# Optimization experiments

Hardware: AMD Instinct MI355X
Metric: run time of the kernel (lower is better)

## Reference

```python
import jax, jax.numpy as jnp
import numpy as np

B, T = 256, 64          # batch, rollout length
D, S, A, E, H = 1024, 64, 32, 1024, 1024  # deter, stoch, action, obs_embed, hidden


def setup_inputs() -> dict:
    key = jax.random.key(0)
    ks = jax.random.split(key, 12)
    f32 = jnp.float32

    def w(k, shape, fan_in):
        return (jax.random.normal(k, shape, f32) / np.float32(np.sqrt(fan_in)))

    return dict(
        obs_embeds=jax.random.normal(ks[0], (B, T, E), f32),
        action_embs=jax.random.normal(ks[1], (B, T, A), f32),
        noise_prior=jax.random.normal(ks[2], (T - 1, B, S), f32),  # randn_like in prior
        noise_post=jax.random.normal(ks[3], (T - 1, B, S), f32),   # randn_like in posterior
        # fc_state_action_embed: Linear(S+A -> D)
        W_sa=w(ks[4], (D, S + A), S + A), b_sa=jnp.zeros((D,), f32),
        # GRUCell(D, D): torch layout [3D, D] with gate order r, z, n
        W_ih=w(ks[5], (3 * D, D), D), b_ih=jnp.zeros((3 * D,), f32),
        W_hh=w(ks[6], (3 * D, D), D), b_hh=jnp.zeros((3 * D,), f32),
        # state_prior: Linear(D->H), ELU, Linear(H->2S)
        Wp1=w(ks[7], (H, D), D), bp1=jnp.zeros((H,), f32),
        Wp2=w(ks[8], (2 * S, H), H), bp2=jnp.zeros((2 * S,), f32),
        # state_posterior: Linear(D+E->H), ELU, Linear(H->2S)
        Wq1=w(ks[9], (H, D + E), D + E), bq1=jnp.zeros((H,), f32),
        Wq2=w(ks[10], (2 * S, H), H), bq2=jnp.zeros((2 * S,), f32),
    )


def reference(obs_embeds, action_embs, noise_prior, noise_post,
              W_sa, b_sa, W_ih, b_ih, W_hh, b_hh,
              Wp1, bp1, Wp2, bp2, Wq1, bq1, Wq2, bq2):
    # observe_rollout: init state is zeros; step t uses obs[:, t+1], action[:, t].
    b = obs_embeds.shape[0]
    h0 = jnp.zeros((b, D), obs_embeds.dtype)
    s0 = jnp.zeros((b, S), obs_embeds.dtype)
    obs_seq = jnp.swapaxes(obs_embeds[:, 1:], 0, 1)   # [T-1, B, E]
    act_seq = jnp.swapaxes(action_embs[:, :-1], 0, 1)  # [T-1, B, A]

    def step(carry, xs):
        h, s = carry  # posterior deter / stoch state from previous step
        obs, act, ep, eq = xs
        # prior: embed (stoch, action) -> GRU update
        e = jax.nn.elu(jnp.concatenate([s, act], -1) @ W_sa.T + b_sa)
        gi = e @ W_ih.T + b_ih
        gh = h @ W_hh.T + b_hh
        ir, iz, ia = jnp.split(gi, 3, axis=-1)
        hr, hz, ha = jnp.split(gh, 3, axis=-1)
        r = jax.nn.sigmoid(ir + hr)
        z = jax.nn.sigmoid(iz + hz)
        n = jnp.tanh(ia + r * ha)
        h_new = (1.0 - z) * n + z * h  # prior deter state
        # prior dist + reparam sample
        pm = jax.nn.elu(h_new @ Wp1.T + bp1) @ Wp2.T + bp2
        pmean, pstd = jnp.split(pm, 2, axis=-1)
        pstd = jax.nn.softplus(pstd) + 0.1
        pstoch = pmean + pstd * ep
        # posterior dist + reparam sample (conditioned on h_new and obs)
        qm = jax.nn.elu(jnp.concatenate([h_new, obs], -1) @ Wq1.T + bq1) @ Wq2.T + bq2
        qmean, qstd = jnp.split(qm, 2, axis=-1)
        qstd = jax.nn.softplus(qstd) + 0.1
        qstoch = qmean + qstd * eq
        out = jnp.concatenate([h_new, pmean, pstd, pstoch, qmean, qstd, qstoch], -1)
        return (h_new, qstoch), out

    _, outs = jax.lax.scan(step, (h0, s0), (obs_seq, act_seq, noise_prior, noise_post))
    # outs: [T-1, B, D + 6S] = (prior deter, prior mean/std/stoch, post mean/std/stoch)
    return outs
```

## Files before the change

### kernel.cpp

```cpp
#include <hip/hip_runtime.h>

typedef __attribute__((ext_vector_type(8))) short short8;
typedef __attribute__((ext_vector_type(4))) float f32x4;

#define OSTEP (256*1408)

#define OFF_WIH  ((size_t)0)
#define OFF_WHH  ((size_t)3145728)
#define OFF_WP1  ((size_t)6291456)
#define OFF_WQ1  ((size_t)7340032)
#define OFF_WP2  ((size_t)9437184)
#define OFF_WQ2  ((size_t)9568256)
#define OFF_HBF0 ((size_t)9699328)
#define OFF_HBF1 ((size_t)9961472)
#define OFF_EBF  ((size_t)10223616)
#define OFF_P1E  ((size_t)10485760)
#define OFF_Q1E  ((size_t)10747904)
#define F32_BYTE_OFF ((size_t)22020096)

__device__ __forceinline__ unsigned short f2bf(float f){
  union { float f; unsigned u; } v; v.f = f;
  unsigned u = v.u;
  u += 0x7fffu + ((u >> 16) & 1u);
  return (unsigned short)(u >> 16);
}
__device__ __forceinline__ float sigf(float x){ return 1.0f/(1.0f+__expf(-x)); }
__device__ __forceinline__ float tanhf_(float x){
  float e = __expf(-2.0f*fabsf(x));
  float t = (1.0f-e)/(1.0f+e);
  return x>=0.f ? t : -t;
}
__device__ __forceinline__ float eluf(float x){ return x>0.f ? x : __expf(x)-1.0f; }
__device__ __forceinline__ float softplusf(float x){ return x>20.f ? x : log1pf(__expf(x)); }
__device__ __forceinline__ short8 ld8(const unsigned short* p){ return *(const short8*)p; }

__global__ void k_prep(const float* __restrict__ wih, const float* __restrict__ whh,
                       const float* __restrict__ wp1, const float* __restrict__ wq1,
                       const float* __restrict__ wp2, const float* __restrict__ wq2,
                       unsigned short* __restrict__ dst){
  size_t i4 = ((size_t)blockIdx.x*256 + threadIdx.x)*4;
  const size_t total = 9699328;
  if(i4 >= total) return;
  const float* src; size_t off;
  if(i4 < 3145728){ src=wih; off=0; }
  else if(i4 < 6291456){ src=whh; off=3145728; }
  else if(i4 < 7340032){ src=wp1; off=6291456; }
  else if(i4 < 9437184){ src=wq1; off=7340032; }
  else if(i4 < 9568256){ src=wp2; off=9437184; }
  else { src=wq2; off=9568256; }
  size_t j = i4 - off;
  float4 v = *(const float4*)(src + j);
  unsigned long long p = (unsigned long long)f2bf(v.x)
                       | ((unsigned long long)f2bf(v.y) << 16)
                       | ((unsigned long long)f2bf(v.z) << 32)
                       | ((unsigned long long)f2bf(v.w) << 48);
  *(unsigned long long*)(dst + i4) = p;
}

__global__ __launch_bounds__(384) void k_gru(
    const unsigned short* __restrict__ e_bf,
    const unsigned short* __restrict__ h_bf,
    const unsigned short* __restrict__ wih_bf,
    const unsigned short* __restrict__ whh_bf,
    const float* __restrict__ b_ih, const float* __restrict__ b_hh,
    const float* __restrict__ hprev, int hprev_ld,
    float* __restrict__ out_t,
    unsigned short* __restrict__ hnext_bf)
{
  int bx = blockIdx.x, by = blockIdx.y;
  int tid = threadIdx.x, w = tid >> 6, lane = tid & 63;
  int g = w % 3; bool isI = (w < 3);
  const unsigned short* A  = isI ? e_bf  : h_bf;
  const unsigned short* Bw = isI ? wih_bf : whh_bf;
  int brow = g*1024 + bx*32;
  int arow = by*32;
  int l15 = lane & 15, q8 = (lane >> 4)*8;

  f32x4 z4 = {0.f,0.f,0.f,0.f};
  f32x4 acc00=z4, acc01=z4, acc10=z4, acc11=z4;

  const unsigned short* pa0 = A  + (size_t)(arow + l15)*1024 + q8;
  const unsigned short* pa1 = pa0 + 16*1024;
  const unsigned short* pb0 = Bw + (size_t)(brow + l15)*1024 + q8;
  const unsigned short* pb1 = pb0 + 16*1024;

  #pragma unroll 4
  for(int kk=0; kk<1024; kk+=32){
    short8 a0 = ld8(pa0+kk), a1 = ld8(pa1+kk);
    short8 b0 = ld8(pb0+kk), b1 = ld8(pb1+kk);
    acc00 = __builtin_amdgcn_mfma_f32_16x16x32_bf16(a0,b0,acc00,0,0,0);
    acc01 = __builtin_amdgcn_mfma_f32_16x16x32_bf16(a0,b1,acc01,0,0,0);
    acc10 = __builtin_amdgcn_mfma_f32_16x16x32_bf16(a1,b0,acc10,0,0,0);
    acc11 = __builtin_amdgcn_mfma_f32_16x16x32_bf16(a1,b1,acc11,0,0,0);
  }

  __shared__ float sg[6][32][33];
  int rr = (lane>>4)*4;
  #pragma unroll
  for(int v=0; v<4; v++){
    sg[w][0 +rr+v][0 +l15] = acc00[v];
    sg[w][0 +rr+v][16+l15] = acc01[v];
    sg[w][16+rr+v][0 +l15] = acc10[v];
    sg[w][16+rr+v][16+l15] = acc11[v];
  }
  __syncthreads();

  for(int i=tid; i<1024; i+=384){
    int m = i>>5, n = i&31;
    int d = bx*32+n, b = by*32+m;
    float ir = sg[0][m][n] + b_ih[d];
    float iz = sg[1][m][n] + b_ih[1024+d];
    float ia = sg[2][m][n] + b_ih[2048+d];
    float hr = sg[3][m][n] + b_hh[d];
    float hz = sg[4][m][n] + b_hh[1024+d];
    float ha = sg[5][m][n] + b_hh[2048+d];
    float r = sigf(ir+hr), zz = sigf(iz+hz);
    float nn = tanhf_(ia + r*ha);
    float hold = hprev[(size_t)b*hprev_ld + d];
    float hnew = (1.f-zz)*nn + zz*hold;
    out_t[(size_t)b*1408 + d] = hnew;
    hnext_bf[(size_t)b*1024 + d] = f2bf(hnew);
  }
}

__global__ __launch_bounds__(256) void k_heads1(
    const unsigned short* __restrict__ hnew_bf,
    const float* __restrict__ obs, int tcol,
    const unsigned short* __restrict__ wp1_bf,
    const unsigned short* __restrict__ wq1_bf,
    const float* __restrict__ bp1, const float* __restrict__ bq1,
    unsigned short* __restrict__ p1e, unsigned short* __restrict__ q1e)
{
  int bx = blockIdx.x, by = blockIdx.y;
  bool isQ = (bx >= 32); int nt = bx & 31;
  int tid = threadIdx.x, w = tid>>6, lane = tid&63;
  int mi = w & 1, ni = w >> 1;
  int l15 = lane & 15, q8 = (lane>>4)*8;
  int arowg = by*32 + mi*16 + l15;
  int browg = nt*32 + ni*16 + l15;

  f32x4 acc = {0.f,0.f,0.f,0.f};
  const unsigned short* pa = hnew_bf + (size_t)arowg*1024 + q8;

  if(!isQ){
    const unsigned short* pb = wp1_bf + (size_t)browg*1024 + q8;
    #pragma unroll 4
    for(int kk=0; kk<1024; kk+=32){
      acc = __builtin_amdgcn_mfma_f32_16x16x32_bf16(ld8(pa+kk), ld8(pb+kk), acc,0,0,0);
    }
  } else {
    const unsigned short* pb = wq1_bf + (size_t)browg*2048 + q8;
    #pragma unroll 4
    for(int kk=0; kk<1024; kk+=32){
      acc = __builtin_amdgcn_mfma_f32_16x16x32_bf16(ld8(pa+kk), ld8(pb+kk), acc,0,0,0);
    }
    const float* obsrow = obs + ((size_t)arowg*64 + tcol)*1024 + q8;
    #pragma unroll 4
    for(int kk=0; kk<1024; kk+=32){
      const float4* f = (const float4*)(obsrow + kk);
      float4 x0 = f[0], x1 = f[1];
      short8 a;
      a[0]=(short)f2bf(x0.x); a[1]=(short)f2bf(x0.y); a[2]=(short)f2bf(x0.z); a[3]=(short)f2bf(x0.w);
      a[4]=(short)f2bf(x1.x); a[5]=(short)f2bf(x1.y); a[6]=(short)f2bf(x1.z); a[7]=(short)f2bf(x1.w);
      acc = __builtin_amdgcn_mfma_f32_16x16x32_bf16(a, ld8(pb+1024+kk), acc,0,0,0);
    }
  }

  const float* bias = isQ ? bq1 : bp1;
  unsigned short* dst = isQ ? q1e : p1e;
  int col = browg;
  float bv = bias[col];
  #pragma unroll
  for(int v=0; v<4; v++){
    int b = by*32 + mi*16 + (lane>>4)*4 + v;
    float val = eluf(acc[v] + bv);
    dst[(size_t)b*1024 + col] = f2bf(val);
  }
}

__global__ __launch_bounds__(256) void k_heads2(
    const unsigned short* __restrict__ p1e, const unsigned short* __restrict__ q1e,
    const unsigned short* __restrict__ wp2_bf, const unsigned short* __restrict__ wq2_bf,
    const float* __restrict__ bp2, const float* __restrict__ bq2,
    float* __restrict__ pm, float* __restrict__ qm)
{
  int bx = blockIdx.x, by = blockIdx.y;
  int col0 = bx*32; bool isQ = (col0 >= 128); int c0 = col0 & 127;
  int tid = threadIdx.x, w = tid>>6, lane = tid&63;
  int mi = w & 1, ni = w >> 1;
  int l15 = lane & 15, q8 = (lane>>4)*8;
  const unsigned short* A  = isQ ? q1e : p1e;
  const unsigned short* Bw = isQ ? wq2_bf : wp2_bf;
  const float* bias = isQ ? bq2 : bp2;
  float* outb = isQ ? qm : pm;

  int arowg = by*32 + mi*16 + l15;
  int browg = c0 + ni*16 + l15;
  f32x4 acc = {0.f,0.f,0.f,0.f};
  const unsigned short* pa = A  + (size_t)arowg*1024 + q8;
  const unsigned short* pb = Bw + (size_t)browg*1024 + q8;
  #pragma unroll 4
  for(int kk=0; kk<1024; kk+=32){
    acc = __builtin_amdgcn_mfma_f32_16x16x32_bf16(ld8(pa+kk), ld8(pb+kk), acc,0,0,0);
  }
  float bv = bias[browg];
  #pragma unroll
  for(int v=0; v<4; v++){
    int b = by*32 + mi*16 + (lane>>4)*4 + v;
    outb[(size_t)b*128 + browg] = acc[v] + bv;
  }
}

__global__ __launch_bounds__(256) void k_sample_e(
    int t_out, int t_act,
    const float* __restrict__ pm, const float* __restrict__ qm,
    const float* __restrict__ noise_p, const float* __restrict__ noise_q,
    const float* __restrict__ act, const float* __restrict__ w_sa,
    const float* __restrict__ b_sa,
    float* __restrict__ out, unsigned short* __restrict__ e_bf)
{
  __shared__ float qst[32*64];
  __shared__ float sact[32*32];
  int bx = blockIdx.x, by = blockIdx.y, tid = threadIdx.x;

  if(t_out >= 0){
    float* out_t = out + (size_t)t_out*OSTEP;
    for(int i=tid; i<2048; i+=256){
      int m = i>>6, s = i&63; int b = by*32+m;
      float qmean = qm[(size_t)b*128 + s];
      float qstd  = softplusf(qm[(size_t)b*128 + 64 + s]) + 0.1f;
      float qs = qmean + qstd * noise_q[((size_t)t_out*256 + b)*64 + s];
      qst[m*64+s] = qs;
      if(bx == 0){
        float pmean = pm[(size_t)b*128 + s];
        float pstd  = softplusf(pm[(size_t)b*128 + 64 + s]) + 0.1f;
        float ps = pmean + pstd * noise_p[((size_t)t_out*256 + b)*64 + s];
        float* o = out_t + (size_t)b*1408;
        o[1024+s] = pmean; o[1088+s] = pstd; o[1152+s] = ps;
        o[1216+s] = qmean; o[1280+s] = qstd; o[1344+s] = qs;
      }
    }
  } else {
    for(int i=tid; i<2048; i+=256) qst[i] = 0.f;
  }
  for(int i=tid; i<1024; i+=256){
    int m = i>>5, k = i&31;
    sact[i] = act[((size_t)(by*32+m)*64 + t_act)*32 + k];
  }
  __syncthreads();

  int n = tid & 31, mb = tid >> 5;
  int d = bx*32 + n;
  const float* wrow = w_sa + (size_t)d*96;
  float a0=b_sa[d], a1=a0, a2=a0, a3=a0;
  for(int k=0; k<64; k++){
    float wv = wrow[k];
    a0 += qst[(mb+ 0)*64+k]*wv;
    a1 += qst[(mb+ 8)*64+k]*wv;
    a2 += qst[(mb+16)*64+k]*wv;
    a3 += qst[(mb+24)*64+k]*wv;
  }
  for(int k=0; k<32; k++){
    float wv = wrow[64+k];
    a0 += sact[(mb+ 0)*32+k]*wv;
    a1 += sact[(mb+ 8)*32+k]*wv;
    a2 += sact[(mb+16)*32+k]*wv;
    a3 += sact[(mb+24)*32+k]*wv;
  }
  e_bf[(size_t)(by*32+mb+ 0)*1024 + d] = f2bf(eluf(a0));
  e_bf[(size_t)(by*32+mb+ 8)*1024 + d] = f2bf(eluf(a1));
  e_bf[(size_t)(by*32+mb+16)*1024 + d] = f2bf(eluf(a2));
  e_bf[(size_t)(by*32+mb+24)*1024 + d] = f2bf(eluf(a3));
}

extern "C" void kernel_launch(void* const* d_in, const int* in_sizes, int n_in,
                              void* d_out, int out_size, void* d_ws, size_t ws_size,
                              hipStream_t stream) {
  const float* obs = (const float*)d_in[0];
  const float* act = (const float*)d_in[1];
  const float* np_ = (const float*)d_in[2];
  const float* nq_ = (const float*)d_in[3];
  const float* wsa = (const float*)d_in[4];
  const float* bsa = (const float*)d_in[5];
  const float* wih = (const float*)d_in[6];
  const float* bih = (const float*)d_in[7];
  const float* whh = (const float*)d_in[8];
  const float* bhh = (const float*)d_in[9];
  const float* wp1 = (const float*)d_in[10];
  const float* bp1 = (const float*)d_in[11];
  const float* wp2 = (const float*)d_in[12];
  const float* bp2 = (const float*)d_in[13];
  const float* wq1 = (const float*)d_in[14];
  const float* bq1 = (const float*)d_in[15];
  const float* wq2 = (const float*)d_in[16];
  const float* bq2 = (const float*)d_in[17];
  float* out = (float*)d_out;

  unsigned short* wsb = (unsigned short*)d_ws;
  unsigned short* wihb = wsb + OFF_WIH;
  unsigned short* whhb = wsb + OFF_WHH;
  unsigned short* wp1b = wsb + OFF_WP1;
  unsigned short* wq1b = wsb + OFF_WQ1;
  unsigned short* wp2b = wsb + OFF_WP2;
  unsigned short* wq2b = wsb + OFF_WQ2;
  unsigned short* hbf0 = wsb + OFF_HBF0;
  unsigned short* hbf1 = wsb + OFF_HBF1;
  unsigned short* ebf  = wsb + OFF_EBF;
  unsigned short* p1e  = wsb + OFF_P1E;
  unsigned short* q1e  = wsb + OFF_Q1E;
  float* f32b = (float*)((char*)d_ws + F32_BYTE_OFF);
  float* h0 = f32b;
  float* pm = f32b + 262144;
  float* qm = f32b + 262144 + 32768;

  hipMemsetAsync(hbf0, 0, 262144*2, stream);
  hipMemsetAsync(h0, 0, 262144*4, stream);

  k_prep<<<9472, 256, 0, stream>>>(wih, whh, wp1, wq1, wp2, wq2, wsb);

  k_sample_e<<<dim3(32,8), 256, 0, stream>>>(-1, 0, pm, qm, np_, nq_, act, wsa, bsa, out, ebf);

  for(int t=0; t<63; t++){
    const unsigned short* hb = (t&1) ? hbf1 : hbf0;
    unsigned short* hbn      = (t&1) ? hbf0 : hbf1;
    const float* hprev = t ? (out + (size_t)(t-1)*OSTEP) : h0;
    int hld = t ? 1408 : 1024;
    k_gru<<<dim3(32,8), 384, 0, stream>>>(ebf, hb, wihb, whhb, bih, bhh,
                                          hprev, hld, out + (size_t)t*OSTEP, hbn);
    k_heads1<<<dim3(64,8), 256, 0, stream>>>(hbn, obs, t+1, wp1b, wq1b, bp1, bq1, p1e, q1e);
    k_heads2<<<dim3(8,8), 256, 0, stream>>>(p1e, q1e, wp2b, wq2b, bp2, bq2, pm, qm);
    k_sample_e<<<dim3(32,8), 256, 0, stream>>>(t, t+1, pm, qm, np_, nq_, act, wsa, bsa, out, ebf);
  }
}
```

Measured before the change: 5.976 ms.

## Fuse rollout into a persistent cooperative kernel with grid-wide syncs

Replaces the per-timestep launches of four kernels (about 250 launches plus prep and memsets) with one persistent cooperative kernel of 256 blocks. Each step runs the GRU, head layer 1, head layer 2 and the sampling/embed phases separated by grid.sync() calls. Weight conversion and zeroing of the initial hidden state are folded into the same kernel. This removes launch overhead and inter-kernel gaps at the cost of grid barriers and a fixed block-to-work mapping, and it falls back to the old multi-kernel path if the cooperative launch fails.

```diff
diff --git a/kernel.cpp b/kernel.cpp
--- a/kernel.cpp
+++ b/kernel.cpp
@@ -1,4 +1,7 @@
 #include <hip/hip_runtime.h>
+#include <hip/hip_cooperative_groups.h>
+
+namespace cg = cooperative_groups;
 
 typedef __attribute__((ext_vector_type(8))) short short8;
 typedef __attribute__((ext_vector_type(4))) float f32x4;
@@ -33,6 +36,296 @@
 __device__ __forceinline__ float eluf(float x){ return x>0.f ? x : __expf(x)-1.0f; }
 __device__ __forceinline__ float softplusf(float x){ return x>20.f ? x : log1pf(__expf(x)); }
 __device__ __forceinline__ short8 ld8(const unsigned short* p){ return *(const short8*)p; }
+
+
+__device__ __forceinline__ void phaseA(
+    int blk, int tid,
+    const unsigned short* __restrict__ e_bf,
+    const unsigned short* __restrict__ h_bf,
+    const unsigned short* __restrict__ wih_bf,
+    const unsigned short* __restrict__ whh_bf,
+    const float* __restrict__ b_ih, const float* __restrict__ b_hh,
+    const float* __restrict__ hprev,
+    float* __restrict__ out_t,
+    unsigned short* __restrict__ hnext_bf,
+    float* sm)
+{
+  float (*sg)[32][33] = (float(*)[32][33])sm;
+  int bx = blk & 31, by = blk >> 5;
+  int w = tid >> 6, lane = tid & 63;
+  if (w < 6) {
+    int g = w % 3; bool isI = (w < 3);
+    const unsigned short* A  = isI ? e_bf  : h_bf;
+    const unsigned short* Bw = isI ? wih_bf : whh_bf;
+    int brow = g*1024 + bx*32;
+    int arow = by*32;
+    int l15 = lane & 15, q8 = (lane >> 4)*8;
+    f32x4 z4 = {0.f,0.f,0.f,0.f};
+    f32x4 acc00=z4, acc01=z4, acc10=z4, acc11=z4;
+    const unsigned short* pa0 = A  + (size_t)(arow + l15)*1024 + q8;
+    const unsigned short* pa1 = pa0 + 16*1024;
+    const unsigned short* pb0 = Bw + (size_t)(brow + l15)*1024 + q8;
+    const unsigned short* pb1 = pb0 + 16*1024;
+    #pragma unroll 4
+    for(int kk=0; kk<1024; kk+=32){
+      short8 a0 = ld8(pa0+kk), a1 = ld8(pa1+kk);
+      short8 b0 = ld8(pb0+kk), b1 = ld8(pb1+kk);
+      acc00 = __builtin_amdgcn_mfma_f32_16x16x32_bf16(a0,b0,acc00,0,0,0);
+      acc01 = __builtin_amdgcn_mfma_f32_16x16x32_bf16(a0,b1,acc01,0,0,0);
+      acc10 = __builtin_amdgcn_mfma_f32_16x16x32_bf16(a1,b0,acc10,0,0,0);
+      acc11 = __builtin_amdgcn_mfma_f32_16x16x32_bf16(a1,b1,acc11,0,0,0);
+    }
+    int rr = (lane>>4)*4;
+    #pragma unroll
+    for(int v=0; v<4; v++){
+      sg[w][0 +rr+v][0 +l15] = acc00[v];
+      sg[w][0 +rr+v][16+l15] = acc01[v];
+      sg[w][16+rr+v][0 +l15] = acc10[v];
+      sg[w][16+rr+v][16+l15] = acc11[v];
+    }
+  }
+  __syncthreads();
+  for(int i=tid; i<1024; i+=512){
+    int m = i>>5, n = i&31;
+    int d = bx*32+n, b = by*32+m;
+    float ir = sg[0][m][n] + b_ih[d];
+    float iz = sg[1][m][n] + b_ih[1024+d];
+    float ia = sg[2][m][n] + b_ih[2048+d];
+    float hr = sg[3][m][n] + b_hh[d];
+    float hz = sg[4][m][n] + b_hh[1024+d];
+    float ha = sg[5][m][n] + b_hh[2048+d];
+    float r = sigf(ir+hr), zz = sigf(iz+hz);
+    float nn = tanhf_(ia + r*ha);
+    float hold = hprev ? hprev[(size_t)b*1408 + d] : 0.f;
+    float hnew = (1.f-zz)*nn + zz*hold;
+    out_t[(size_t)b*1408 + d] = hnew;
+    hnext_bf[(size_t)b*1024 + d] = f2bf(hnew);
+  }
+}
+
+__device__ __forceinline__ void phaseB(
+    int blk, int tid,
+    const unsigned short* __restrict__ hnew_bf,
+    const float* __restrict__ obs, int tcol,
+    const unsigned short* __restrict__ wp1_bf,
+    const unsigned short* __restrict__ wq1_bf,
+    const float* __restrict__ bp1, const float* __restrict__ bq1,
+    unsigned short* __restrict__ p1e, unsigned short* __restrict__ q1e)
+{
+  int w = tid >> 6, lane = tid & 63;
+  int vb = blk*2 + (w>>2);
+  int bx = vb & 63, by = vb >> 6;
+  bool isQ = (bx >= 32); int nt = bx & 31;
+  int w4 = w & 3;
+  int mi = w4 & 1, ni = w4 >> 1;
+  int l15 = lane & 15, q8 = (lane>>4)*8;
+  int arowg = by*32 + mi*16 + l15;
+  int browg = nt*32 + ni*16 + l15;
+
+  f32x4 acc = {0.f,0.f,0.f,0.f};
+  const unsigned short* pa = hnew_bf + (size_t)arowg*1024 + q8;
+
+  if(!isQ){
+    const unsigned short* pb = wp1_bf + (size_t)browg*1024 + q8;
+    #pragma unroll 4
+    for(int kk=0; kk<1024; kk+=32){
+      acc = __builtin_amdgcn_mfma_f32_16x16x32_bf16(ld8(pa+kk), ld8(pb+kk), acc,0,0,0);
+    }
+  } else {
+    const unsigned short* pb = wq1_bf + (size_t)browg*2048 + q8;
+    #pragma unroll 4
+    for(int kk=0; kk<1024; kk+=32){
+      acc = __builtin_amdgcn_mfma_f32_16x16x32_bf16(ld8(pa+kk), ld8(pb+kk), acc,0,0,0);
+    }
+    const float* obsrow = obs + ((size_t)arowg*64 + tcol)*1024 + q8;
+    #pragma unroll 4
+    for(int kk=0; kk<1024; kk+=32){
+      const float4* f = (const float4*)(obsrow + kk);
+      float4 x0 = f[0], x1 = f[1];
+      short8 a;
+      a[0]=(short)f2bf(x0.x); a[1]=(short)f2bf(x0.y); a[2]=(short)f2bf(x0.z); a[3]=(short)f2bf(x0.w);
+      a[4]=(short)f2bf(x1.x); a[5]=(short)f2bf(x1.y); a[6]=(short)f2bf(x1.z); a[7]=(short)f2bf(x1.w);
+      acc = __builtin_amdgcn_mfma_f32_16x16x32_bf16(a, ld8(pb+1024+kk), acc,0,0,0);
+    }
+  }
+
+  const float* bias = isQ ? bq1 : bp1;
+  unsigned short* dst = isQ ? q1e : p1e;
+  int col = browg;
+  float bv = bias[col];
+  #pragma unroll
+  for(int v=0; v<4; v++){
+    int b = by*32 + mi*16 + (lane>>4)*4 + v;
+    float val = eluf(acc[v] + bv);
+    dst[(size_t)b*1024 + col] = f2bf(val);
+  }
+}
+
+__device__ __forceinline__ void phaseC(
+    int blk, int tid,
+    const unsigned short* __restrict__ p1e, const unsigned short* __restrict__ q1e,
+    const unsigned short* __restrict__ wp2_bf, const unsigned short* __restrict__ wq2_bf,
+    const float* __restrict__ bp2, const float* __restrict__ bq2,
+    float* __restrict__ pm, float* __restrict__ qm)
+{
+  if (tid >= 64) return;
+  int by = blk >> 5, bx = (blk >> 2) & 7, w4 = blk & 3;
+  int lane = tid;
+  int col0 = bx*32; bool isQ = (col0 >= 128); int c0 = col0 & 127;
+  int mi = w4 & 1, ni = w4 >> 1;
+  int l15 = lane & 15, q8 = (lane>>4)*8;
+  const unsigned short* A  = isQ ? q1e : p1e;
+  const unsigned short* Bw = isQ ? wq2_bf : wp2_bf;
+  const float* bias = isQ ? bq2 : bp2;
+  float* outb = isQ ? qm : pm;
+
+  int arowg = by*32 + mi*16 + l15;
+  int browg = c0 + ni*16 + l15;
+  f32x4 acc = {0.f,0.f,0.f,0.f};
+  const unsigned short* pa = A  + (size_t)arowg*1024 + q8;
+  const unsigned short* pb = Bw + (size_t)browg*1024 + q8;
+  #pragma unroll 4
+  for(int kk=0; kk<1024; kk+=32){
+    acc = __builtin_amdgcn_mfma_f32_16x16x32_bf16(ld8(pa+kk), ld8(pb+kk), acc,0,0,0);
+  }
+  float bv = bias[browg];
+  #pragma unroll
+  for(int v=0; v<4; v++){
+    int b = by*32 + mi*16 + (lane>>4)*4 + v;
+    outb[(size_t)b*128 + browg] = acc[v] + bv;
+  }
+}
+
+__device__ __forceinline__ void phaseD(
+    int t_out, int t_act, int blk, int tid,
+    const float* __restrict__ pm, const float* __restrict__ qm,
+    const float* __restrict__ noise_p, const float* __restrict__ noise_q,
+    const float* __restrict__ act, const float* __restrict__ w_sa,
+    const float* __restrict__ b_sa,
+    float* __restrict__ out, unsigned short* __restrict__ e_bf,
+    float* sm)
+{
+  float* qst  = sm;
+  float* sact = sm + 2048;
+  int bx = blk & 31, by = blk >> 5;
+
+  if(t_out >= 0){
+    float* out_t = out + (size_t)t_out*OSTEP;
+    for(int i=tid; i<2048; i+=512){
+      int m = i>>6, s = i&63; int b = by*32+m;
+      float qmean = qm[(size_t)b*128 + s];
+      float qstd  = softplusf(qm[(size_t)b*128 + 64 + s]) + 0.1f;
+      float qs = qmean + qstd * noise_q[((size_t)t_out*256 + b)*64 + s];
+      qst[m*64+s] = qs;
+      if(bx == 0){
+        float pmean = pm[(size_t)b*128 + s];
+        float pstd  = softplusf(pm[(size_t)b*128 + 64 + s]) + 0.1f;
+        float ps = pmean + pstd * noise_p[((size_t)t_out*256 + b)*64 + s];
+        float* o = out_t + (size_t)b*1408;
+        o[1024+s] = pmean; o[1088+s] = pstd; o[1152+s] = ps;
+        o[1216+s] = qmean; o[1280+s] = qstd; o[1344+s] = qs;
+      }
+    }
+  } else {
+    for(int i=tid; i<2048; i+=512) qst[i] = 0.f;
+  }
+  for(int i=tid; i<1024; i+=512){
+    int m = i>>5, k = i&31;
+    sact[i] = act[((size_t)(by*32+m)*64 + t_act)*32 + k];
+  }
+  __syncthreads();
+
+  int n = tid & 31, mb = tid >> 5;
+  int d = bx*32 + n;
+  const float* wrow = w_sa + (size_t)d*96;
+  float a0=b_sa[d], a1=a0;
+  for(int k=0; k<64; k++){
+    float wv = wrow[k];
+    a0 += qst[(mb+ 0)*64+k]*wv;
+    a1 += qst[(mb+16)*64+k]*wv;
+  }
+  for(int k=0; k<32; k++){
+    float wv = wrow[64+k];
+    a0 += sact[(mb+ 0)*32+k]*wv;
+    a1 += sact[(mb+16)*32+k]*wv;
+  }
+  e_bf[(size_t)(by*32+mb+ 0)*1024 + d] = f2bf(eluf(a0));
+  e_bf[(size_t)(by*32+mb+16)*1024 + d] = f2bf(eluf(a1));
+}
+
+__global__ __launch_bounds__(512, 1) void k_mega(
+    const float* __restrict__ obs, const float* __restrict__ act,
+    const float* __restrict__ np_, const float* __restrict__ nq_,
+    const float* __restrict__ wsa, const float* __restrict__ bsa,
+    const float* __restrict__ wih, const float* __restrict__ bih,
+    const float* __restrict__ whh, const float* __restrict__ bhh,
+    const float* __restrict__ wp1, const float* __restrict__ bp1,
+    const float* __restrict__ wp2, const float* __restrict__ bp2,
+    const float* __restrict__ wq1, const float* __restrict__ bq1,
+    const float* __restrict__ wq2, const float* __restrict__ bq2,
+    float* __restrict__ out, unsigned short* __restrict__ wsb)
+{
+  __shared__ float sm[6*32*33];
+  cg::grid_group grid = cg::this_grid();
+  int blk = blockIdx.x, tid = threadIdx.x;
+
+  unsigned short* wihb = wsb + OFF_WIH;
+  unsigned short* whhb = wsb + OFF_WHH;
+  unsigned short* wp1b = wsb + OFF_WP1;
+  unsigned short* wq1b = wsb + OFF_WQ1;
+  unsigned short* wp2b = wsb + OFF_WP2;
+  unsigned short* wq2b = wsb + OFF_WQ2;
+  unsigned short* hbf0 = wsb + OFF_HBF0;
+  unsigned short* hbf1 = wsb + OFF_HBF1;
+  unsigned short* ebf  = wsb + OFF_EBF;
+  unsigned short* p1e  = wsb + OFF_P1E;
+  unsigned short* q1e  = wsb + OFF_Q1E;
+  float* f32b = (float*)((char*)wsb + F32_BYTE_OFF);
+  float* pm = f32b + 262144;
+  float* qm = f32b + 262144 + 32768;
+
+  {
+    size_t gtid = (size_t)blk*512 + tid;
+    for(size_t i = gtid; i < (size_t)2424832; i += (size_t)131072){
+      size_t i4 = i*4;
+      const float* src; size_t off;
+      if(i4 < 3145728){ src=wih; off=0; }
+      else if(i4 < 6291456){ src=whh; off=3145728; }
+      else if(i4 < 7340032){ src=wp1; off=6291456; }
+      else if(i4 < 9437184){ src=wq1; off=7340032; }
+      else if(i4 < 9568256){ src=wp2; off=9437184; }
+      else { src=wq2; off=9568256; }
+      size_t j = i4 - off;
+      float4 v = *(const float4*)(src + j);
+      unsigned long long p = (unsigned long long)f2bf(v.x)
+                           | ((unsigned long long)f2bf(v.y) << 16)
+                           | ((unsigned long long)f2bf(v.z) << 32)
+                           | ((unsigned long long)f2bf(v.w) << 48);
+      *(unsigned long long*)(wsb + i4) = p;
+    }
+    if(gtid < 65536) ((unsigned long long*)(wsb + OFF_HBF0))[gtid] = 0ull;
+  }
+  phaseD(-1, 0, blk, tid, pm, qm, np_, nq_, act, wsa, bsa, out, ebf, sm);
+  grid.sync();
+
+  #pragma unroll 1
+  for(int t=0; t<63; t++){
+    const unsigned short* hb = (t&1) ? hbf1 : hbf0;
+    unsigned short* hbn      = (t&1) ? hbf0 : hbf1;
+    const float* hprev = t ? (out + (size_t)(t-1)*OSTEP) : (const float*)nullptr;
+
+    phaseA(blk, tid, ebf, hb, wihb, whhb, bih, bhh, hprev,
+           out + (size_t)t*OSTEP, hbn, sm);
+    grid.sync();
+    phaseB(blk, tid, hbn, obs, t+1, wp1b, wq1b, bp1, bq1, p1e, q1e);
+    grid.sync();
+    phaseC(blk, tid, p1e, q1e, wp2b, wq2b, bp2, bq2, pm, qm);
+    grid.sync();
+    phaseD(t, t+1, blk, tid, pm, qm, np_, nq_, act, wsa, bsa, out, ebf, sm);
+    grid.sync();
+  }
+}
+
 
 __global__ void k_prep(const float* __restrict__ wih, const float* __restrict__ whh,
                        const float* __restrict__ wp1, const float* __restrict__ wq1,
@@ -295,8 +588,20 @@
   const float* wq2 = (const float*)d_in[16];
   const float* bq2 = (const float*)d_in[17];
   float* out = (float*)d_out;
-
   unsigned short* wsb = (unsigned short*)d_ws;
+
+  void* args[] = {
+    (void*)&obs, (void*)&act, (void*)&np_, (void*)&nq_,
+    (void*)&wsa, (void*)&bsa, (void*)&wih, (void*)&bih,
+    (void*)&whh, (void*)&bhh, (void*)&wp1, (void*)&bp1,
+    (void*)&wp2, (void*)&bp2, (void*)&wq1, (void*)&bq1,
+    (void*)&wq2, (void*)&bq2, (void*)&out, (void*)&wsb
+  };
+  hipError_t err = hipLaunchCooperativeKernel((const void*)k_mega,
+                                              dim3(256), dim3(512),
+                                              args, 0, stream);
+  if (err == hipSuccess) return;
+
   unsigned short* wihb = wsb + OFF_WIH;
   unsigned short* whhb = wsb + OFF_WHH;
   unsigned short* wp1b = wsb + OFF_WP1;
@@ -317,7 +622,6 @@
   hipMemsetAsync(h0, 0, 262144*4, stream);
 
   k_prep<<<9472, 256, 0, stream>>>(wih, whh, wp1, wq1, wp2, wq2, wsb);
-
   k_sample_e<<<dim3(32,8), 256, 0, stream>>>(-1, 0, pm, qm, np_, nq_, act, wsa, bsa, out, ebf);
 
   for(int t=0; t<63; t++){
```

After: 12.67 ms. 2.12x slower.

## Fuse the rollout into one persistent cooperative kernel with LDS-resident weights

Applied to the files above, without the earlier changes.

Replaces the per-timestep launches of four kernels with one cooperative persistent kernel of 256 blocks. Each block converts its slice of every weight matrix to bf16 once and keeps it in LDS for all 63 steps. Phases are separated by an atomic-counter grid barrier. This removes launch overhead and repeated global weight reads. In exchange it adds grid-wide barrier latency four times per step, gives each phase narrow per-block work, and uses a bounded spin that could break correctness if the barrier times out.

```diff
diff --git a/kernel.cpp b/kernel.cpp
--- a/kernel.cpp
+++ b/kernel.cpp
@@ -2,6 +2,7 @@
 
 typedef __attribute__((ext_vector_type(8))) short short8;
 typedef __attribute__((ext_vector_type(4))) float f32x4;
+typedef unsigned short us;
 
 #define OSTEP (256*1408)
 
@@ -18,6 +19,14 @@
 #define OFF_Q1E  ((size_t)10747904)
 #define F32_BYTE_OFF ((size_t)22020096)
 
+#define L_WAI 0
+#define L_WAH 24576
+#define L_WB  49152
+#define L_WC  73728
+#define L_WD  77824
+#define L_SCR 79488
+#define LDS_TOTAL 129664
+
 __device__ __forceinline__ unsigned short f2bf(float f){
   union { float f; unsigned u; } v; v.f = f;
   unsigned u = v.u;
@@ -32,12 +41,274 @@
 }
 __device__ __forceinline__ float eluf(float x){ return x>0.f ? x : __expf(x)-1.0f; }
 __device__ __forceinline__ float softplusf(float x){ return x>20.f ? x : log1pf(__expf(x)); }
-__device__ __forceinline__ short8 ld8(const unsigned short* p){ return *(const short8*)p; }
+__device__ __forceinline__ short8 ld8(const us* p){ return *(const short8*)p; }
+
+
+__device__ __forceinline__ void phaseA_new(
+    char* lds, int blk, int tid, int t,
+    const us* __restrict__ ebf, const us* __restrict__ hb, us* __restrict__ hbn,
+    const float* __restrict__ b_ih, const float* __restrict__ b_hh,
+    const float* __restrict__ hprev, float* __restrict__ out_t,
+    const float* __restrict__ obs, us* __restrict__ obsbf)
+{
+  int w = tid>>6, lane = tid&63;
+  int l15 = lane&15, q8 = (lane>>4)*8;
+  int xr = (l15&7)<<4;
+  const char* wbi = lds + L_WAI + l15*2048;
+  const char* wbh = lds + L_WAH + l15*2048;
+  const us* paE = ebf + (size_t)(w*32 + l15)*1024 + q8;
+  const us* paH = hb  + (size_t)(w*32 + l15)*1024 + q8;
+  f32x4 z={0.f,0.f,0.f,0.f}, aI0=z, aI1=z, aH0=z, aH1=z;
+  #pragma unroll 4
+  for(int kk=0; kk<1024; kk+=32){
+    int kb = (kk+q8)*2;
+    short8 bI = *(const short8*)(wbi + (kb^xr));
+    short8 bH = *(const short8*)(wbh + (kb^xr));
+    short8 e0 = ld8(paE+kk), e1 = ld8(paE+16384+kk);
+    short8 h0 = ld8(paH+kk), h1 = ld8(paH+16384+kk);
+    aI0 = __builtin_amdgcn_mfma_f32_16x16x32_bf16(e0,bI,aI0,0,0,0);
+    aI1 = __builtin_amdgcn_mfma_f32_16x16x32_bf16(e1,bI,aI1,0,0,0);
+    aH0 = __builtin_amdgcn_mfma_f32_16x16x32_bf16(h0,bH,aH0,0,0,0);
+    aH1 = __builtin_amdgcn_mfma_f32_16x16x32_bf16(h1,bH,aH1,0,0,0);
+  }
+  float* Gih = (float*)(lds + L_SCR);
+  float* Ghh = Gih + 16*257;
+  int rr = (lane>>4)*4;
+  #pragma unroll
+  for(int v=0; v<4; v++){
+    Gih[l15*257 + w*32 + rr + v]      = aI0[v];
+    Gih[l15*257 + w*32 + 16 + rr + v] = aI1[v];
+    Ghh[l15*257 + w*32 + rr + v]      = aH0[v];
+    Ghh[l15*257 + w*32 + 16 + rr + v] = aH1[v];
+  }
+  {
+    const float* src = obs + ((size_t)(blk*64) + (t+1))*1024;
+    us* dst = obsbf + (size_t)blk*1024;
+    for(int i=tid;i<1024;i+=512) dst[i] = f2bf(src[i]);
+  }
+  __syncthreads();
+  for(int i=tid;i<1024;i+=512){
+    int di=i>>8, b=i&255; int d=blk*4+di;
+    float ir = Gih[(di  )*257 + b] + b_ih[d];
+    float iz = Gih[(4+di)*257 + b] + b_ih[1024+d];
+    float ia = Gih[(8+di)*257 + b] + b_ih[2048+d];
+    float hr = Ghh[(di  )*257 + b] + b_hh[d];
+    float hz = Ghh[(4+di)*257 + b] + b_hh[1024+d];
+    float ha = Ghh[(8+di)*257 + b] + b_hh[2048+d];
+    float r = sigf(ir+hr), zz = sigf(iz+hz);
+    float nn = tanhf_(ia + r*ha);
+    float hold = hprev ? hprev[(size_t)b*1408 + d] : 0.f;
+    float hnew = (1.f-zz)*nn + zz*hold;
+    out_t[(size_t)b*1408 + d] = hnew;
+    hbn[(size_t)b*1024 + d] = f2bf(hnew);
+  }
+}
+
+__device__ __forceinline__ void phaseB_new(
+    char* lds, int blk, int tid,
+    const us* __restrict__ hbn, const us* __restrict__ obsbf,
+    const float* __restrict__ bp1, const float* __restrict__ bq1,
+    us* __restrict__ p1e, us* __restrict__ q1e)
+{
+  int w=tid>>6, lane=tid&63, l15=lane&15, q8=(lane>>4)*8, xr=(l15&7)<<4;
+  const char* wb = lds + L_WB + l15*2048;
+  const us* paH = hbn   + (size_t)(w*32+l15)*1024 + q8;
+  const us* paO = obsbf + (size_t)(w*32+l15)*1024 + q8;
+  f32x4 z={0.f,0.f,0.f,0.f}, c10=z,c11=z,c20=z,c21=z;
+  #pragma unroll 4
+  for(int kk=0;kk<1024;kk+=32){
+    int kb=(kk+q8)*2;
+    short8 bw = *(const short8*)(wb + (kb^xr));
+    c10 = __builtin_amdgcn_mfma_f32_16x16x32_bf16(ld8(paH+kk),       bw, c10,0,0,0);
+    c11 = __builtin_amdgcn_mfma_f32_16x16x32_bf16(ld8(paH+16384+kk), bw, c11,0,0,0);
+    c20 = __builtin_amdgcn_mfma_f32_16x16x32_bf16(ld8(paO+kk),       bw, c20,0,0,0);
+    c21 = __builtin_amdgcn_mfma_f32_16x16x32_bf16(ld8(paO+16384+kk), bw, c21,0,0,0);
+  }
+  float* G1 = (float*)(lds+L_SCR); float* G2 = G1 + 16*257;
+  int rr=(lane>>4)*4;
+  #pragma unroll
+  for(int v=0;v<4;v++){
+    G1[l15*257 + w*32 + rr + v]      = c10[v];
+    G1[l15*257 + w*32 + 16 + rr + v] = c11[v];
+    G2[l15*257 + w*32 + rr + v]      = c20[v];
+    G2[l15*257 + w*32 + 16 + rr + v] = c21[v];
+  }
+  __syncthreads();
+  for(int i=tid;i<1024;i+=512){
+    int ci=i>>8, b=i&255; int c=blk*4+ci;
+    float p1 = eluf(G1[ci*257+b] + bp1[c]);
+    float q1 = eluf(G1[(4+ci)*257+b] + G2[(8+ci)*257+b] + bq1[c]);
+    p1e[(size_t)b*1024+c]=f2bf(p1);
+    q1e[(size_t)b*1024+c]=f2bf(q1);
+  }
+}
+
+__device__ __forceinline__ void phaseC_new(
+    char* lds, int blk, int tid, int t,
+    const us* __restrict__ p1e, const us* __restrict__ q1e,
+    const float* __restrict__ bp2, const float* __restrict__ bq2,
+    const float* __restrict__ np_, const float* __restrict__ nq_,
+    float* __restrict__ out_t, float* __restrict__ qstg)
+{
+  int w=tid>>6, lane=tid&63, l15=lane&15, q8=(lane>>4)*8, xr=(l15&7)<<4;
+  int kind = blk>>7, idx=blk&127, s=idx>>1, bh=idx&1, b0=bh*128;
+  const us* A = kind ? q1e : p1e;
+  const char* wc = lds + L_WC + l15*2048;
+  const us* pa = A + (size_t)(b0 + w*16 + l15)*1024 + q8;
+  f32x4 c0={0.f,0.f,0.f,0.f};
+  #pragma unroll 4
+  for(int kk=0;kk<1024;kk+=32){
+    int kb=(kk+q8)*2;
+    c0 = __builtin_amdgcn_mfma_f32_16x16x32_bf16(ld8(pa+kk), *(const short8*)(wc+(kb^xr)), c0,0,0,0);
+  }
+  float* Gc=(float*)(lds+L_SCR);
+  int rr=(lane>>4)*4;
+  #pragma unroll
+  for(int v=0;v<4;v++) Gc[l15*129 + w*16 + rr + v] = c0[v];
+  __syncthreads();
+  const float* b2 = kind? bq2 : bp2;
+  const float* nz = kind? nq_ : np_;
+  if(tid<128){
+    int b=tid, bg=b0+b;
+    float mean = Gc[0*129+b] + b2[s];
+    float stdv = softplusf(Gc[1*129+b] + b2[64+s]) + 0.1f;
+    float st = mean + stdv * nz[((size_t)t*256+bg)*64 + s];
+    float* o = out_t + (size_t)bg*1408 + (kind?1216:1024);
+    o[s]=mean; o[64+s]=stdv; o[128+s]=st;
+    if(kind) qstg[(size_t)bg*64+s]=st;
+  }
+}
+
+__device__ __forceinline__ void phaseD_new(
+    char* lds, int blk, int tid, int t_out, int t_act,
+    const float* __restrict__ qstg, const float* __restrict__ act,
+    const float* __restrict__ b_sa, us* __restrict__ ebf)
+{
+  float* wd  = (float*)(lds + L_WD);
+  float* qld = (float*)(lds + L_SCR);
+  float* ald = qld + 128*65;
+  int dl = tid>>7, b = tid&127;
+  int d = blk*4 + dl;
+  float bias = b_sa[d];
+  for(int ch=0; ch<2; ch++){
+    int B0 = ch*128;
+    if(t_out>=0){
+      for(int i=tid;i<8192;i+=512){int bb=i>>6,k=i&63; qld[bb*65+k]=qstg[(size_t)(B0+bb)*64+k];}
+    } else {
+      for(int i=tid;i<8192;i+=512){int bb=i>>6,k=i&63; qld[bb*65+k]=0.f;}
+    }
+    for(int i=tid;i<4096;i+=512){int bb=i>>5,k=i&31; ald[bb*33+k]=act[((size_t)(B0+bb)*64 + t_act)*32 + k];}
+    __syncthreads();
+    float a = bias;
+    for(int k=0;k<64;k++) a += qld[b*65+k]*wd[dl*96+k];
+    for(int k=0;k<32;k++) a += ald[b*33+k]*wd[dl*96+64+k];
+    ebf[(size_t)(B0+b)*1024 + d] = f2bf(eluf(a));
+    __syncthreads();
+  }
+}
+
+__global__ __launch_bounds__(512, 1) void k_mega(
+    const float* __restrict__ obs, const float* __restrict__ act,
+    const float* __restrict__ np_, const float* __restrict__ nq_,
+    const float* __restrict__ wsa, const float* __restrict__ bsa,
+    const float* __restrict__ wih, const float* __restrict__ bih,
+    const float* __restrict__ whh, const float* __restrict__ bhh,
+    const float* __restrict__ wp1, const float* __restrict__ bp1,
+    const float* __restrict__ wp2, const float* __restrict__ bp2,
+    const float* __restrict__ wq1, const float* __restrict__ bq1,
+    const float* __restrict__ wq2, const float* __restrict__ bq2,
+    float* __restrict__ out, us* __restrict__ wsb)
+{
+  extern __shared__ char lds[];
+  int blk = blockIdx.x, tid = threadIdx.x;
+
+  us* obsbf = wsb + OFF_WIH;
+  us* hbf0  = wsb + OFF_HBF0;
+  us* hbf1  = wsb + OFF_HBF1;
+  us* ebf   = wsb + OFF_EBF;
+  us* p1e   = wsb + OFF_P1E;
+  us* q1e   = wsb + OFF_Q1E;
+  float* f32b = (float*)((char*)wsb + F32_BYTE_OFF);
+  unsigned* cnt = (unsigned*)f32b;
+  float* qstg = f32b + 8192;
+
+  unsigned ep = 0;
+  #define GBAR() do{ __syncthreads(); ++ep; \
+    if(tid==0){ \
+      __hip_atomic_fetch_add(cnt,1u,__ATOMIC_RELEASE,__HIP_MEMORY_SCOPE_AGENT); \
+      unsigned _it=0; \
+      while(__hip_atomic_load(cnt,__ATOMIC_RELAXED,__HIP_MEMORY_SCOPE_AGENT) < ep*256u \
+            && _it<65536u){ ++_it; __builtin_amdgcn_s_sleep(2); } \
+      (void)__hip_atomic_load(cnt,__ATOMIC_ACQUIRE,__HIP_MEMORY_SCOPE_AGENT); \
+    } \
+    __syncthreads(); }while(0)
+
+  for(int i=tid; i<12*512; i+=512){
+    int r=i>>9, kp=(i&511)*2;
+    int srow = (r>>2)*1024 + blk*4 + (r&3);
+    float2 vI = *(const float2*)(wih + (size_t)srow*1024 + kp);
+    float2 vH = *(const float2*)(whh + (size_t)srow*1024 + kp);
+    unsigned pI = (unsigned)f2bf(vI.x) | ((unsigned)f2bf(vI.y)<<16);
+    unsigned pH = (unsigned)f2bf(vH.x) | ((unsigned)f2bf(vH.y)<<16);
+    int off = r*2048 + ((kp*2)^((r&7)<<4));
+    *(unsigned*)(lds + L_WAI + off) = pI;
+    *(unsigned*)(lds + L_WAH + off) = pH;
+  }
+  for(int i=tid; i<12*512; i+=512){
+    int r=i>>9, kp=(i&511)*2;
+    const float* src;
+    if(r<4)      src = wp1 + (size_t)(blk*4+r)*1024 + kp;
+    else if(r<8) src = wq1 + (size_t)(blk*4+r-4)*2048 + kp;
+    else         src = wq1 + (size_t)(blk*4+r-8)*2048 + 1024 + kp;
+    float2 v = *(const float2*)src;
+    unsigned p = (unsigned)f2bf(v.x) | ((unsigned)f2bf(v.y)<<16);
+    *(unsigned*)(lds + L_WB + r*2048 + ((kp*2)^((r&7)<<4))) = p;
+  }
+  {
+    int kind=blk>>7, s=(blk&127)>>1;
+    const float* W2 = kind? wq2 : wp2;
+    for(int i=tid; i<2*512; i+=512){
+      int r=i>>9, kp=(i&511)*2;
+      float2 v = *(const float2*)(W2 + (size_t)((r?64:0)+s)*1024 + kp);
+      unsigned p = (unsigned)f2bf(v.x) | ((unsigned)f2bf(v.y)<<16);
+      *(unsigned*)(lds + L_WC + r*2048 + ((kp*2)^((r&7)<<4))) = p;
+    }
+  }
+  for(int i=tid;i<384;i+=512){
+    int r=i/96, k=i-r*96;
+    ((float*)(lds+L_WD))[r*96+k] = wsa[(size_t)(blk*4+r)*96 + k];
+  }
+  { unsigned long long* p=(unsigned long long*)hbf0;
+    for(int i=tid;i<256;i+=512) p[(size_t)blk*256+i]=0ull; }
+  __syncthreads();
+
+  phaseD_new(lds, blk, tid, -1, 0, qstg, act, bsa, ebf);
+  GBAR();
+
+  #pragma unroll 1
+  for(int t=0; t<63; t++){
+    const us* hb = (t&1) ? hbf1 : hbf0;
+    us* hbn      = (t&1) ? hbf0 : hbf1;
+    const float* hprev = t ? (out + (size_t)(t-1)*OSTEP) : (const float*)nullptr;
+    float* out_t = out + (size_t)t*OSTEP;
+
+    phaseA_new(lds, blk, tid, t, ebf, hb, hbn, bih, bhh, hprev, out_t, obs, obsbf);
+    GBAR();
+    phaseB_new(lds, blk, tid, hbn, obsbf, bp1, bq1, p1e, q1e);
+    GBAR();
+    phaseC_new(lds, blk, tid, t, p1e, q1e, bp2, bq2, np_, nq_, out_t, qstg);
+    GBAR();
+    phaseD_new(lds, blk, tid, t, t+1, qstg, act, bsa, ebf);
+    GBAR();
+  }
+  #undef GBAR
+}
+
 
 __global__ void k_prep(const float* __restrict__ wih, const float* __restrict__ whh,
                        const float* __restrict__ wp1, const float* __restrict__ wq1,
                        const float* __restrict__ wp2, const float* __restrict__ wq2,
-                       unsigned short* __restrict__ dst){
+                       us* __restrict__ dst){
   size_t i4 = ((size_t)blockIdx.x*256 + threadIdx.x)*4;
   const size_t total = 9699328;
   if(i4 >= total) return;
@@ -58,20 +329,17 @@
 }
 
 __global__ __launch_bounds__(384) void k_gru(
-    const unsigned short* __restrict__ e_bf,
-    const unsigned short* __restrict__ h_bf,
-    const unsigned short* __restrict__ wih_bf,
-    const unsigned short* __restrict__ whh_bf,
+    const us* __restrict__ e_bf, const us* __restrict__ h_bf,
+    const us* __restrict__ wih_bf, const us* __restrict__ whh_bf,
     const float* __restrict__ b_ih, const float* __restrict__ b_hh,
     const float* __restrict__ hprev, int hprev_ld,
-    float* __restrict__ out_t,
-    unsigned short* __restrict__ hnext_bf)
+    float* __restrict__ out_t, us* __restrict__ hnext_bf)
 {
   int bx = blockIdx.x, by = blockIdx.y;
   int tid = threadIdx.x, w = tid >> 6, lane = tid & 63;
   int g = w % 3; bool isI = (w < 3);
-  const unsigned short* A  = isI ? e_bf  : h_bf;
-  const unsigned short* Bw = isI ? wih_bf : whh_bf;
+  const us* A  = isI ? e_bf  : h_bf;
+  const us* Bw = isI ? wih_bf : whh_bf;
   int brow = g*1024 + bx*32;
   int arow = by*32;
   int l15 = lane & 15, q8 = (lane >> 4)*8;
@@ -79,10 +347,10 @@
   f32x4 z4 = {0.f,0.f,0.f,0.f};
   f32x4 acc00=z4, acc01=z4, acc10=z4, acc11=z4;
 
-  const unsigned short* pa0 = A  + (size_t)(arow + l15)*1024 + q8;
-  const unsigned short* pa1 = pa0 + 16*1024;
-  const unsigned short* pb0 = Bw + (size_t)(brow + l15)*1024 + q8;
-  const unsigned short* pb1 = pb0 + 16*1024;
+  const us* pa0 = A  + (size_t)(arow + l15)*1024 + q8;
+  const us* pa1 = pa0 + 16*1024;
+  const us* pb0 = Bw + (size_t)(brow + l15)*1024 + q8;
+  const us* pb1 = pb0 + 16*1024;
 
   #pragma unroll 4
   for(int kk=0; kk<1024; kk+=32){
@@ -124,12 +392,11 @@
 }
 
 __global__ __launch_bounds__(256) void k_heads1(
-    const unsigned short* __restrict__ hnew_bf,
+    const us* __restrict__ hnew_bf,
     const float* __restrict__ obs, int tcol,
-    const unsigned short* __restrict__ wp1_bf,
-    const unsigned short* __restrict__ wq1_bf,
+    const us* __restrict__ wp1_bf, const us* __restrict__ wq1_bf,
     const float* __restrict__ bp1, const float* __restrict__ bq1,
-    unsigned short* __restrict__ p1e, unsigned short* __restrict__ q1e)
+    us* __restrict__ p1e, us* __restrict__ q1e)
 {
   int bx = blockIdx.x, by = blockIdx.y;
   bool isQ = (bx >= 32); int nt = bx & 31;
@@ -140,16 +407,16 @@
   int browg = nt*32 + ni*16 + l15;
 
   f32x4 acc = {0.f,0.f,0.f,0.f};
-  const unsigned short* pa = hnew_bf + (size_t)arowg*1024 + q8;
+  const us* pa = hnew_bf + (size_t)arowg*1024 + q8;
 
   if(!isQ){
-    const unsigned short* pb = wp1_bf + (size_t)browg*1024 + q8;
+    const us* pb = wp1_bf + (size_t)browg*1024 + q8;
     #pragma unroll 4
     for(int kk=0; kk<1024; kk+=32){
       acc = __builtin_amdgcn_mfma_f32_16x16x32_bf16(ld8(pa+kk), ld8(pb+kk), acc,0,0,0);
     }
   } else {
-    const unsigned short* pb = wq1_bf + (size_t)browg*2048 + q8;
+    const us* pb = wq1_bf + (size_t)browg*2048 + q8;
     #pragma unroll 4
     for(int kk=0; kk<1024; kk+=32){
       acc = __builtin_amdgcn_mfma_f32_16x16x32_bf16(ld8(pa+kk), ld8(pb+kk), acc,0,0,0);
@@ -167,7 +434,7 @@
   }
 
   const float* bias = isQ ? bq1 : bp1;
-  unsigned short* dst = isQ ? q1e : p1e;
+  us* dst = isQ ? q1e : p1e;
   int col = browg;
   float bv = bias[col];
   #pragma unroll
@@ -179,8 +446,8 @@
 }
 
 __global__ __launch_bounds__(256) void k_heads2(
-    const unsigned short* __restrict__ p1e, const unsigned short* __restrict__ q1e,
-    const unsigned short* __restrict__ wp2_bf, const unsigned short* __restrict__ wq2_bf,
+    const us* __restrict__ p1e, const us* __restrict__ q1e,
+    const us* __restrict__ wp2_bf, const us* __restrict__ wq2_bf,
     const float* __restrict__ bp2, const float* __restrict__ bq2,
     float* __restrict__ pm, float* __restrict__ qm)
 {
@@ -189,16 +456,16 @@
   int tid = threadIdx.x, w = tid>>6, lane = tid&63;
   int mi = w & 1, ni = w >> 1;
   int l15 = lane & 15, q8 = (lane>>4)*8;
-  const unsigned short* A  = isQ ? q1e : p1e;
-  const unsigned short* Bw = isQ ? wq2_bf : wp2_bf;
+  const us* A  = isQ ? q1e : p1e;
+  const us* Bw = isQ ? wq2_bf : wp2_bf;
   const float* bias = isQ ? bq2 : bp2;
   float* outb = isQ ? qm : pm;
 
   int arowg = by*32 + mi*16 + l15;
   int browg = c0 + ni*16 + l15;
   f32x4 acc = {0.f,0.f,0.f,0.f};
-  const unsigned short* pa = A  + (size_t)arowg*1024 + q8;
-  const unsigned short* pb = Bw + (size_t)browg*1024 + q8;
+  const us* pa = A  + (size_t)arowg*1024 + q8;
+  const us* pb = Bw + (size_t)browg*1024 + q8;
   #pragma unroll 4
   for(int kk=0; kk<1024; kk+=32){
     acc = __builtin_amdgcn_mfma_f32_16x16x32_bf16(ld8(pa+kk), ld8(pb+kk), acc,0,0,0);
@@ -217,7 +484,7 @@
     const float* __restrict__ noise_p, const float* __restrict__ noise_q,
     const float* __restrict__ act, const float* __restrict__ w_sa,
     const float* __restrict__ b_sa,
-    float* __restrict__ out, unsigned short* __restrict__ e_bf)
+    float* __restrict__ out, us* __restrict__ e_bf)
 {
   __shared__ float qst[32*64];
   __shared__ float sact[32*32];
@@ -295,19 +562,41 @@
   const float* wq2 = (const float*)d_in[16];
   const float* bq2 = (const float*)d_in[17];
   float* out = (float*)d_out;
-
-  unsigned short* wsb = (unsigned short*)d_ws;
-  unsigned short* wihb = wsb + OFF_WIH;
-  unsigned short* whhb = wsb + OFF_WHH;
-  unsigned short* wp1b = wsb + OFF_WP1;
-  unsigned short* wq1b = wsb + OFF_WQ1;
-  unsigned short* wp2b = wsb + OFF_WP2;
-  unsigned short* wq2b = wsb + OFF_WQ2;
-  unsigned short* hbf0 = wsb + OFF_HBF0;
-  unsigned short* hbf1 = wsb + OFF_HBF1;
-  unsigned short* ebf  = wsb + OFF_EBF;
-  unsigned short* p1e  = wsb + OFF_P1E;
-  unsigned short* q1e  = wsb + OFF_Q1E;
+  us* wsb = (us*)d_ws;
+
+  hipMemsetAsync((char*)d_ws + F32_BYTE_OFF, 0, 1152, stream);
+
+  static int lds_ok = -1;
+  if (lds_ok < 0) {
+    hipError_t e = hipFuncSetAttribute((const void*)k_mega,
+                     hipFuncAttributeMaxDynamicSharedMemorySize, LDS_TOTAL);
+    lds_ok = (e == hipSuccess) ? 1 : 0;
+  }
+  if (lds_ok == 1) {
+    void* args[] = {
+      (void*)&obs, (void*)&act, (void*)&np_, (void*)&nq_,
+      (void*)&wsa, (void*)&bsa, (void*)&wih, (void*)&bih,
+      (void*)&whh, (void*)&bhh, (void*)&wp1, (void*)&bp1,
+      (void*)&wp2, (void*)&bp2, (void*)&wq1, (void*)&bq1,
+      (void*)&wq2, (void*)&bq2, (void*)&out, (void*)&wsb
+    };
+    hipError_t err = hipLaunchCooperativeKernel((const void*)k_mega,
+                                                dim3(256), dim3(512),
+                                                args, LDS_TOTAL, stream);
+    if (err == hipSuccess) return;
+  }
+
+  us* wihb = wsb + OFF_WIH;
+  us* whhb = wsb + OFF_WHH;
+  us* wp1b = wsb + OFF_WP1;
+  us* wq1b = wsb + OFF_WQ1;
+  us* wp2b = wsb + OFF_WP2;
+  us* wq2b = wsb + OFF_WQ2;
+  us* hbf0 = wsb + OFF_HBF0;
+  us* hbf1 = wsb + OFF_HBF1;
+  us* ebf  = wsb + OFF_EBF;
+  us* p1e  = wsb + OFF_P1E;
+  us* q1e  = wsb + OFF_Q1E;
   float* f32b = (float*)((char*)d_ws + F32_BYTE_OFF);
   float* h0 = f32b;
   float* pm = f32b + 262144;
@@ -317,12 +606,11 @@
   hipMemsetAsync(h0, 0, 262144*4, stream);
 
   k_prep<<<9472, 256, 0, stream>>>(wih, whh, wp1, wq1, wp2, wq2, wsb);
-
   k_sample_e<<<dim3(32,8), 256, 0, stream>>>(-1, 0, pm, qm, np_, nq_, act, wsa, bsa, out, ebf);
 
   for(int t=0; t<63; t++){
-    const unsigned short* hb = (t&1) ? hbf1 : hbf0;
-    unsigned short* hbn      = (t&1) ? hbf0 : hbf1;
+    const us* hb = (t&1) ? hbf1 : hbf0;
+    us* hbn      = (t&1) ? hbf0 : hbf1;
     const float* hprev = t ? (out + (size_t)(t-1)*OSTEP) : h0;
     int hld = t ? 1408 : 1024;
     k_gru<<<dim3(32,8), 384, 0, stream>>>(ebf, hb, wihb, whhb, bih, bhh,
```

Measured after the change: 12.08 ms. +102.1%, slower.
